# Performance work log

Hardware: AMD Instinct MI355X
Metric: run time of the kernel (lower is better)

Reference implementation:

```python
import jax, jax.numpy as jnp
import numpy as np

B, T, C = 128, 256, 384
H, HD = 8, 48          # num_heads, head_dim
WINDOW = 64

def setup_inputs() -> dict:
    key = jax.random.key(0)
    ks = jax.random.split(key, 5)
    return {
        "x": jax.random.normal(ks[0], (B, T, C), dtype=jnp.float32),
        "W_qkv": jax.random.normal(ks[1], (C, 3 * C), dtype=jnp.float32) * (1.0 / np.sqrt(C)),
        "b_qkv": jax.random.normal(ks[2], (3 * C,), dtype=jnp.float32) * 0.02,
        "W_proj": jax.random.normal(ks[3], (C, C), dtype=jnp.float32) * (1.0 / np.sqrt(C)),
        "b_proj": jax.random.normal(ks[4], (C,), dtype=jnp.float32) * 0.02,
        "gate": jnp.ones((C,), dtype=jnp.float32),
    }

def reference(x, W_qkv, b_qkv, W_proj, b_proj, gate):
    Bx, Tx, Cx = x.shape
    qkv = x @ W_qkv + b_qkv                                   # [B,T,3C]
    q, k, v = jnp.split(qkv, 3, axis=-1)
    q = q.reshape(Bx, Tx, H, HD).transpose(0, 2, 1, 3)        # [B,H,T,hd]
    k = k.reshape(Bx, Tx, H, HD).transpose(0, 2, 1, 3)
    v = v.reshape(Bx, Tx, H, HD).transpose(0, 2, 1, 3)
    scale = 1.0 / np.sqrt(HD).astype(np.float32)
    att = jnp.einsum("bhqd,bhkd->bhqk", q, k) * scale        # [B,H,T,T]
    idx = jnp.arange(Tx)
    causal = idx[:, None] >= idx[None, :]                     # lower-tri
    local = jnp.abs(idx[None, :] - idx[:, None]) <= WINDOW
    mask = (causal & local)[None, None, :, :]
    att = jnp.where(mask, att, -jnp.inf)
    att = jax.nn.softmax(att, axis=-1)
    out = jnp.einsum("bhqk,bhkd->bhqd", att, v)               # [B,H,T,hd]
    out = out.transpose(0, 2, 1, 3).reshape(Bx, Tx, Cx)       # [B,T,C]
    return (out * gate) @ W_proj + b_proj
```

## Files before the change

kernel.cpp:

```cpp
#include <hip/hip_runtime.h>
#include <hip/hip_bf16.h>

typedef __attribute__((ext_vector_type(8))) short bf16x8;
typedef __attribute__((ext_vector_type(4))) float floatx4;

#define NB 128
#define NT 256
#define NC 384
#define NH 8
#define ND 48

static __device__ __forceinline__ unsigned short f2bf(float f) {
  __hip_bfloat16 h = __float2bfloat16(f);
  return __builtin_bit_cast(unsigned short, h);
}

static __device__ __forceinline__ void gload16(const unsigned short* g, unsigned short* l) {
  __builtin_amdgcn_global_load_lds(
      (const __attribute__((address_space(1))) void*)g,
      (__attribute__((address_space(3))) void*)l, 16, 0, 0);
}

__global__ __launch_bounds__(256) void k_prep(const float* __restrict__ x,
                                              const float* __restrict__ Wq,
                                              const float* __restrict__ Wp,
                                              unsigned short* __restrict__ xbf,
                                              unsigned short* __restrict__ WqT,
                                              unsigned short* __restrict__ WpT) {
  const int blk = blockIdx.x;
  const int t = threadIdx.x;
  if (blk < 144) {
    __shared__ float T[64][65];
    const float* src;
    unsigned short* dst;
    int N, kt, nt;
    if (blk < 108) { src = Wq; dst = WqT; N = 1152; kt = blk / 18; nt = blk % 18; }
    else { int b2 = blk - 108; src = Wp; dst = WpT; N = 384; kt = b2 / 6; nt = b2 % 6; }
    const int k0 = kt * 64, n0 = nt * 64;
    const int r = t >> 2, c = (t & 3) * 16;
    const float* s = src + (size_t)(k0 + r) * N + n0 + c;
#pragma unroll
    for (int i = 0; i < 4; ++i) *(float4*)&T[r][c + i * 4] = ((const float4*)s)[i];
    __syncthreads();
    unsigned short o[16];
#pragma unroll
    for (int i = 0; i < 16; ++i) o[i] = f2bf(T[c + i][r]);
    unsigned short* dp = dst + (size_t)(n0 + r) * 384 + k0 + c;
    *(bf16x8*)dp = *(bf16x8*)&o[0];
    *(bf16x8*)(dp + 8) = *(bf16x8*)&o[8];
  } else {
    const int n8 = (NB * NT * NC) / 8;
    int idx = (blk - 144) * 256 + t;
    const int stride = (gridDim.x - 144) * 256;
    for (; idx < n8; idx += stride) {
      const float* s = x + (size_t)idx * 8;
      float v[8];
      *(float4*)&v[0] = ((const float4*)s)[0];
      *(float4*)&v[4] = ((const float4*)s)[1];
      bf16x8 p;
#pragma unroll
      for (int i = 0; i < 8; ++i) p[i] = f2bf(v[i]);
      *(bf16x8*)(xbf + (size_t)idx * 8) = p;
    }
  }
}

#define STAGE_G(Ag, Bg, As, Bs, k0, buf)                                             \
  {                                                                                  \
    const int r0_ = (lane >> 2), sw0_ = 8 * ((lane & 3) ^ ((r0_ >> 1) & 3));         \
    const int r1_ = r0_ + 16,    sw1_ = 8 * ((lane & 3) ^ ((r1_ >> 1) & 3));         \
    gload16(Ag + (size_t)r0_ * 384 + (k0) + sw0_, As + (buf)*4096 + (w * 32) * 32);  \
    gload16(Ag + (size_t)r1_ * 384 + (k0) + sw1_, As + (buf)*4096 + (w * 32 + 16) * 32); \
    gload16(Bg + (size_t)r0_ * 384 + (k0) + sw0_, Bs + (buf)*4096 + (w * 32) * 32);  \
    gload16(Bg + (size_t)r1_ * 384 + (k0) + sw1_, Bs + (buf)*4096 + (w * 32 + 16) * 32); \
  }

#define GEMM_PIPE(Ag, Bg, As, Bs)                                                    \
  STAGE_G(Ag, Bg, As, Bs, 0, 0);                                                     \
  STAGE_G(Ag, Bg, As, Bs, 32, 1);                                                    \
  _Pragma("unroll") for (int t_ = 0; t_ < 12; ++t_) {                                \
    if (t_ < 11) asm volatile("s_waitcnt vmcnt(4)" ::: "memory");                    \
    else         asm volatile("s_waitcnt vmcnt(0)" ::: "memory");                    \
    __builtin_amdgcn_s_barrier();                                                    \
    if (t_ < 10) STAGE_G(Ag, Bg, As, Bs, (t_ + 2) * 32, (t_ + 2) % 3);               \
    const unsigned short* Ac_ = As + (t_ % 3) * 4096;                                \
    const unsigned short* Bc_ = Bs + (t_ % 3) * 4096;                                \
    bf16x8 a_[4], b_[4];                                                             \
    _Pragma("unroll") for (int mt = 0; mt < 4; ++mt) {                               \
      const int R = wm * 64 + mt * 16 + lq;                                          \
      a_[mt] = *(const bf16x8*)&Ac_[R * 32 + 8 * (lg ^ ((R >> 1) & 3))];             \
    }                                                                                \
    _Pragma("unroll") for (int nt = 0; nt < 4; ++nt) {                               \
      const int R = wn * 64 + nt * 16 + lq;                                          \
      b_[nt] = *(const bf16x8*)&Bc_[R * 32 + 8 * (lg ^ ((R >> 1) & 3))];             \
    }                                                                                \
    _Pragma("unroll") for (int mt = 0; mt < 4; ++mt)                                 \
      _Pragma("unroll") for (int nt = 0; nt < 4; ++nt)                               \
        acc[mt][nt] = __builtin_amdgcn_mfma_f32_16x16x32_bf16(a_[mt], b_[nt], acc[mt][nt], 0, 0, 0); \
  }

__global__ __launch_bounds__(256) void k_qkv(const unsigned short* __restrict__ xb,
                                             const unsigned short* __restrict__ WqT,
                                             const float* __restrict__ bq,
                                             unsigned short* __restrict__ qkv) {
  __shared__ __align__(16) unsigned short As[3 * 128 * 32];
  __shared__ __align__(16) unsigned short Bs[3 * 128 * 32];
  const int t = threadIdx.x, lane = t & 63, w = t >> 6;
  const int wm = w >> 1, wn = w & 1;
  const int lq = lane & 15, lg = lane >> 4;
  const int m0 = blockIdx.x * 128, n0 = blockIdx.y * 128;
  const unsigned short* Ag = xb + (size_t)(m0 + w * 32) * 384;
  const unsigned short* Bg = WqT + (size_t)(n0 + w * 32) * 384;
  floatx4 acc[4][4] = {};

  GEMM_PIPE(Ag, Bg, As, Bs);

  const int comp = n0 / 384;
  const int cb = n0 - comp * 384;
#pragma unroll
  for (int nt = 0; nt < 4; ++nt) {
    const int cc = cb + wn * 64 + nt * 16 + lq;
    const int h = cc / 48, d = cc - h * 48;
    const float bias = bq[n0 + wn * 64 + nt * 16 + lq];
#pragma unroll
    for (int mt = 0; mt < 4; ++mt) {
#pragma unroll
      for (int j = 0; j < 4; ++j) {
        const int row = m0 + wm * 64 + mt * 16 + lg * 4 + j;
        const int bb = row >> 8, tt = row & 255;
        qkv[((((size_t)comp * NB + bb) * NH + h) * NT + tt) * ND + d] =
            f2bf(acc[mt][nt][j] + bias);
      }
    }
  }
}

__global__ __launch_bounds__(256) void k_proj(const unsigned short* __restrict__ A,
                                              const unsigned short* __restrict__ WpT,
                                              const float* __restrict__ bp,
                                              float* __restrict__ out) {
  __shared__ __align__(16) unsigned short As[3 * 128 * 32];
  __shared__ __align__(16) unsigned short Bs[3 * 128 * 32];
  const int t = threadIdx.x, lane = t & 63, w = t >> 6;
  const int wm = w >> 1, wn = w & 1;
  const int lq = lane & 15, lg = lane >> 4;
  const int m0 = blockIdx.x * 128, n0 = blockIdx.y * 128;
  const unsigned short* Ag = A + (size_t)(m0 + w * 32) * 384;
  const unsigned short* Bg = WpT + (size_t)(n0 + w * 32) * 384;
  floatx4 acc[4][4] = {};

  GEMM_PIPE(Ag, Bg, As, Bs);

#pragma unroll
  for (int nt = 0; nt < 4; ++nt) {
    const int col = n0 + wn * 64 + nt * 16 + lq;
    const float bias = bp[col];
#pragma unroll
    for (int mt = 0; mt < 4; ++mt)
#pragma unroll
      for (int j = 0; j < 4; ++j) {
        const int row = m0 + wm * 64 + mt * 16 + lg * 4 + j;
        out[(size_t)row * 384 + col] = acc[mt][nt][j] + bias;
      }
  }
}

__global__ __launch_bounds__(256) void k_attn(const unsigned short* __restrict__ qkv,
                                              const float* __restrict__ gate,
                                              unsigned short* __restrict__ attg) {
  __shared__ __align__(16) unsigned short Ks[128 * 72];
  __shared__ __align__(16) unsigned short Vt[48 * 152];
  __shared__ __align__(16) unsigned short Ps[4 * 16 * 104];
  const int t = threadIdx.x;
  const int blk = blockIdx.x;
  const int tile = blk & 3;
  const int bh = blk >> 2;
  const int b = bh >> 3, h = bh & 7;
  const int base = tile * 64;
  const size_t kvoff = (size_t)bh * NT * ND;
  const unsigned short* qptr = qkv + kvoff;
  const unsigned short* kptr = qkv + (size_t)NB * NH * NT * ND + kvoff;
  const unsigned short* vptr = qkv + (size_t)2 * NB * NH * NT * ND + kvoff;

  if (t < 48) {
    bf16x8 z = {};
    *(bf16x8*)&Vt[t * 152 + 128] = z;
    *(bf16x8*)&Vt[t * 152 + 136] = z;
  }
  if (t < 128) {
    const int r = t, ka = base - 64 + r;
    unsigned short* dst = &Ks[r * 72];
    if (ka >= 0) {
      const unsigned short* src = kptr + (size_t)ka * ND;
#pragma unroll
      for (int i = 0; i < 6; ++i) *(bf16x8*)(dst + i * 8) = *(const bf16x8*)(src + i * 8);
      bf16x8 z = {};
      *(bf16x8*)(dst + 48) = z;
      *(bf16x8*)(dst + 56) = z;
    } else {
      bf16x8 z = {};
#pragma unroll
      for (int i = 0; i < 8; ++i) *(bf16x8*)(dst + i * 8) = z;
    }
  } else {
    const int r = t - 128, ka = base - 64 + r;
    if (ka >= 0) {
      const unsigned short* src = vptr + (size_t)ka * ND;
      bf16x8 vv[6];
#pragma unroll
      for (int i = 0; i < 6; ++i) vv[i] = *(const bf16x8*)(src + i * 8);
#pragma unroll
      for (int i = 0; i < 6; ++i)
#pragma unroll
        for (int j = 0; j < 8; ++j)
          Vt[(i * 8 + j) * 152 + r] = (unsigned short)vv[i][j];
    } else {
#pragma unroll
      for (int d = 0; d < 48; ++d) Vt[d * 152 + r] = 0;
    }
  }
  __syncthreads();

  const int lane = t & 63, w = t >> 6;
  const int lq = lane & 15, lg = lane >> 4;
  const int qs = base + w * 16;

  const unsigned short* qrow = qptr + (size_t)(qs + lq) * ND;
  bf16x8 aq0 = *(const bf16x8*)(qrow + lg * 8);
  bf16x8 aq1 = {};
  if (lg < 2) aq1 = *(const bf16x8*)(qrow + 32 + lg * 8);

  floatx4 s[5];
#pragma unroll
  for (int kt = 0; kt < 5; ++kt) {
    const unsigned short* kr = &Ks[(w * 16 + kt * 16 + lq) * 72];
    bf16x8 kb0 = *(const bf16x8*)(kr + lg * 8);
    bf16x8 kb1 = *(const bf16x8*)(kr + 32 + lg * 8);
    floatx4 z = {};
    z = __builtin_amdgcn_mfma_f32_16x16x32_bf16(aq0, kb0, z, 0, 0, 0);
    z = __builtin_amdgcn_mfma_f32_16x16x32_bf16(aq1, kb1, z, 0, 0, 0);
    s[kt] = z;
  }

  const float scale = 0.14433756729740643f;
  floatx4 pj[5];
#pragma unroll
  for (int j = 0; j < 4; ++j) {
    const int qa = qs + lg * 4 + j;
    float mx = -1e30f;
    float sv[5];
    bool ok[5];
#pragma unroll
    for (int kt = 0; kt < 5; ++kt) {
      const int ka = base - 64 + w * 16 + kt * 16 + lq;
      sv[kt] = s[kt][j] * scale;
      ok[kt] = (ka >= 0) && (ka <= qa) && (qa - ka <= 64);
      if (ok[kt]) mx = fmaxf(mx, sv[kt]);
    }
#pragma unroll
    for (int dd = 1; dd < 16; dd <<= 1) mx = fmaxf(mx, __shfl_xor(mx, dd));
    float sum = 0.f;
#pragma unroll
    for (int kt = 0; kt < 5; ++kt) {
      float p = ok[kt] ? __expf(sv[kt] - mx) : 0.f;
      pj[kt][j] = p;
      sum += p;
    }
#pragma unroll
    for (int dd = 1; dd < 16; dd <<= 1) sum += __shfl_xor(sum, dd);
    const float inv = 1.f / sum;
#pragma unroll
    for (int kt = 0; kt < 5; ++kt) pj[kt][j] *= inv;
  }

  unsigned short* pw = &Ps[w * 16 * 104];
#pragma unroll
  for (int kt = 0; kt < 5; ++kt)
#pragma unroll
    for (int j = 0; j < 4; ++j)
      pw[(lg * 4 + j) * 104 + kt * 16 + lq] = f2bf(pj[kt][j]);
#pragma unroll
  for (int j = 0; j < 4; ++j) pw[lq * 104 + 80 + lg * 4 + j] = 0;

  floatx4 o[3] = {};
#pragma unroll
  for (int c = 0; c < 3; ++c) {
    bf16x8 ap = *(const bf16x8*)&pw[lq * 104 + c * 32 + lg * 8];
#pragma unroll
    for (int nt = 0; nt < 3; ++nt) {
      bf16x8 av = *(const bf16x8*)&Vt[(nt * 16 + lq) * 152 + w * 16 + c * 32 + lg * 8];
      o[nt] = __builtin_amdgcn_mfma_f32_16x16x32_bf16(ap, av, o[nt], 0, 0, 0);
    }
  }
#pragma unroll
  for (int nt = 0; nt < 3; ++nt) {
    const int d = nt * 16 + lq;
    const int c = h * ND + d;
    const float g = gate[c];
#pragma unroll
    for (int j = 0; j < 4; ++j) {
      const int tt = qs + lg * 4 + j;
      attg[((size_t)b * NT + tt) * NC + c] = f2bf(o[nt][j] * g);
    }
  }
}

extern "C" void kernel_launch(void* const* d_in, const int* in_sizes, int n_in,
                              void* d_out, int out_size, void* d_ws, size_t ws_size,
                              hipStream_t stream) {
  const float* x    = (const float*)d_in[0];
  const float* Wq   = (const float*)d_in[1];
  const float* bq   = (const float*)d_in[2];
  const float* Wp   = (const float*)d_in[3];
  const float* bp   = (const float*)d_in[4];
  const float* gate = (const float*)d_in[5];

  const size_t nx = (size_t)NB * NT * NC;
  unsigned short* attg = (unsigned short*)d_ws;
  unsigned short* xbf  = attg + nx;
  unsigned short* qkvp = xbf + nx;
  unsigned short* WqT  = qkvp + (size_t)3 * NB * NH * NT * ND;
  unsigned short* WpT  = WqT + (size_t)384 * 1152;
  float* out = (float*)d_out;

  k_prep<<<dim3(1680), 256, 0, stream>>>(x, Wq, Wp, xbf, WqT, WpT);
  k_qkv<<<dim3(256, 9), 256, 0, stream>>>(xbf, WqT, bq, qkvp);
  k_attn<<<dim3(4096), 256, 0, stream>>>(qkvp, gate, attg);
  k_proj<<<dim3(256, 3), 256, 0, stream>>>(attg, WpT, bp, out);
}
```

Baseline: 117.7 us.

## Deepen GEMM pipeline, store QKV row-major, fold gate into projection weights

The shared GEMM pipeline goes from three to four LDS stages, with one extra prefetch in flight and wave priority raised around the MFMA block. The QKV epilogue now writes a plain row-major [B*T,1152] layout instead of scattering into per-head tensors, and the attention kernel reads Q/K/V with a 1152 stride. The gate multiply moves from the attention epilogue into the projection weight transpose in k_prep. These target vmem latency stalls and scattered stores, at the cost of more LDS per block (possible occupancy loss) and strided attention loads.

New measurement: 137.1 us. +16.5%, slower.

```diff
diff --git a/kernel.cpp b/kernel.cpp
--- a/kernel.cpp
+++ b/kernel.cpp
@@ -24,6 +24,7 @@
 __global__ __launch_bounds__(256) void k_prep(const float* __restrict__ x,
                                               const float* __restrict__ Wq,
                                               const float* __restrict__ Wp,
+                                              const float* __restrict__ gate,
                                               unsigned short* __restrict__ xbf,
                                               unsigned short* __restrict__ WqT,
                                               unsigned short* __restrict__ WpT) {
@@ -34,7 +35,8 @@
     const float* src;
     unsigned short* dst;
     int N, kt, nt;
-    if (blk < 108) { src = Wq; dst = WqT; N = 1152; kt = blk / 18; nt = blk % 18; }
+    const bool isWp = (blk >= 108);
+    if (!isWp) { src = Wq; dst = WqT; N = 1152; kt = blk / 18; nt = blk % 18; }
     else { int b2 = blk - 108; src = Wp; dst = WpT; N = 384; kt = b2 / 6; nt = b2 % 6; }
     const int k0 = kt * 64, n0 = nt * 64;
     const int r = t >> 2, c = (t & 3) * 16;
@@ -42,9 +44,17 @@
 #pragma unroll
     for (int i = 0; i < 4; ++i) *(float4*)&T[r][c + i * 4] = ((const float4*)s)[i];
     __syncthreads();
+    float gv[16];
+    if (isWp) {
+#pragma unroll
+      for (int i = 0; i < 4; ++i) *(float4*)&gv[i * 4] = ((const float4*)(gate + k0 + c))[i];
+    } else {
+#pragma unroll
+      for (int i = 0; i < 16; ++i) gv[i] = 1.f;
+    }
     unsigned short o[16];
 #pragma unroll
-    for (int i = 0; i < 16; ++i) o[i] = f2bf(T[c + i][r]);
+    for (int i = 0; i < 16; ++i) o[i] = f2bf(T[c + i][r] * gv[i]);
     unsigned short* dp = dst + (size_t)(n0 + r) * 384 + k0 + c;
     *(bf16x8*)dp = *(bf16x8*)&o[0];
     *(bf16x8*)(dp + 8) = *(bf16x8*)&o[8];
@@ -78,13 +88,15 @@
 #define GEMM_PIPE(Ag, Bg, As, Bs)                                                    \
   STAGE_G(Ag, Bg, As, Bs, 0, 0);                                                     \
   STAGE_G(Ag, Bg, As, Bs, 32, 1);                                                    \
+  STAGE_G(Ag, Bg, As, Bs, 64, 2);                                                    \
   _Pragma("unroll") for (int t_ = 0; t_ < 12; ++t_) {                                \
-    if (t_ < 11) asm volatile("s_waitcnt vmcnt(4)" ::: "memory");                    \
-    else         asm volatile("s_waitcnt vmcnt(0)" ::: "memory");                    \
+    if (t_ <= 9)       asm volatile("s_waitcnt vmcnt(8)" ::: "memory");              \
+    else if (t_ == 10) asm volatile("s_waitcnt vmcnt(4)" ::: "memory");              \
+    else               asm volatile("s_waitcnt vmcnt(0)" ::: "memory");              \
     __builtin_amdgcn_s_barrier();                                                    \
-    if (t_ < 10) STAGE_G(Ag, Bg, As, Bs, (t_ + 2) * 32, (t_ + 2) % 3);               \
-    const unsigned short* Ac_ = As + (t_ % 3) * 4096;                                \
-    const unsigned short* Bc_ = Bs + (t_ % 3) * 4096;                                \
+    if (t_ < 9) STAGE_G(Ag, Bg, As, Bs, (t_ + 3) * 32, (t_ + 3) & 3);                \
+    const unsigned short* Ac_ = As + (t_ & 3) * 4096;                                \
+    const unsigned short* Bc_ = Bs + (t_ & 3) * 4096;                                \
     bf16x8 a_[4], b_[4];                                                             \
     _Pragma("unroll") for (int mt = 0; mt < 4; ++mt) {                               \
       const int R = wm * 64 + mt * 16 + lq;                                          \
@@ -94,17 +106,19 @@
       const int R = wn * 64 + nt * 16 + lq;                                          \
       b_[nt] = *(const bf16x8*)&Bc_[R * 32 + 8 * (lg ^ ((R >> 1) & 3))];             \
     }                                                                                \
+    __builtin_amdgcn_s_setprio(1);                                                   \
     _Pragma("unroll") for (int mt = 0; mt < 4; ++mt)                                 \
       _Pragma("unroll") for (int nt = 0; nt < 4; ++nt)                               \
         acc[mt][nt] = __builtin_amdgcn_mfma_f32_16x16x32_bf16(a_[mt], b_[nt], acc[mt][nt], 0, 0, 0); \
+    __builtin_amdgcn_s_setprio(0);                                                   \
   }
 
 __global__ __launch_bounds__(256) void k_qkv(const unsigned short* __restrict__ xb,
                                              const unsigned short* __restrict__ WqT,
                                              const float* __restrict__ bq,
                                              unsigned short* __restrict__ qkv) {
-  __shared__ __align__(16) unsigned short As[3 * 128 * 32];
-  __shared__ __align__(16) unsigned short Bs[3 * 128 * 32];
+  __shared__ __align__(16) unsigned short As[4 * 128 * 32];
+  __shared__ __align__(16) unsigned short Bs[4 * 128 * 32];
   const int t = threadIdx.x, lane = t & 63, w = t >> 6;
   const int wm = w >> 1, wn = w & 1;
   const int lq = lane & 15, lg = lane >> 4;
@@ -115,23 +129,17 @@
 
   GEMM_PIPE(Ag, Bg, As, Bs);
 
-  const int comp = n0 / 384;
-  const int cb = n0 - comp * 384;
 #pragma unroll
   for (int nt = 0; nt < 4; ++nt) {
-    const int cc = cb + wn * 64 + nt * 16 + lq;
-    const int h = cc / 48, d = cc - h * 48;
-    const float bias = bq[n0 + wn * 64 + nt * 16 + lq];
-#pragma unroll
-    for (int mt = 0; mt < 4; ++mt) {
+    const int col = n0 + wn * 64 + nt * 16 + lq;
+    const float bias = bq[col];
+#pragma unroll
+    for (int mt = 0; mt < 4; ++mt)
 #pragma unroll
       for (int j = 0; j < 4; ++j) {
         const int row = m0 + wm * 64 + mt * 16 + lg * 4 + j;
-        const int bb = row >> 8, tt = row & 255;
-        qkv[((((size_t)comp * NB + bb) * NH + h) * NT + tt) * ND + d] =
-            f2bf(acc[mt][nt][j] + bias);
+        qkv[(size_t)row * 1152 + col] = f2bf(acc[mt][nt][j] + bias);
       }
-    }
   }
 }
 
@@ -139,8 +147,8 @@
                                               const unsigned short* __restrict__ WpT,
                                               const float* __restrict__ bp,
                                               float* __restrict__ out) {
-  __shared__ __align__(16) unsigned short As[3 * 128 * 32];
-  __shared__ __align__(16) unsigned short Bs[3 * 128 * 32];
+  __shared__ __align__(16) unsigned short As[4 * 128 * 32];
+  __shared__ __align__(16) unsigned short Bs[4 * 128 * 32];
   const int t = threadIdx.x, lane = t & 63, w = t >> 6;
   const int wm = w >> 1, wn = w & 1;
   const int lq = lane & 15, lg = lane >> 4;
@@ -166,7 +174,6 @@
 }
 
 __global__ __launch_bounds__(256) void k_attn(const unsigned short* __restrict__ qkv,
-                                              const float* __restrict__ gate,
                                               unsigned short* __restrict__ attg) {
   __shared__ __align__(16) unsigned short Ks[128 * 72];
   __shared__ __align__(16) unsigned short Vt[48 * 152];
@@ -177,10 +184,9 @@
   const int bh = blk >> 2;
   const int b = bh >> 3, h = bh & 7;
   const int base = tile * 64;
-  const size_t kvoff = (size_t)bh * NT * ND;
-  const unsigned short* qptr = qkv + kvoff;
-  const unsigned short* kptr = qkv + (size_t)NB * NH * NT * ND + kvoff;
-  const unsigned short* vptr = qkv + (size_t)2 * NB * NH * NT * ND + kvoff;
+  const unsigned short* qbase = qkv + (size_t)(b * NT) * 1152 + h * 48;
+  const unsigned short* kbase = qbase + 384;
+  const unsigned short* vbase = qbase + 768;
 
   if (t < 48) {
     bf16x8 z = {};
@@ -191,7 +197,7 @@
     const int r = t, ka = base - 64 + r;
     unsigned short* dst = &Ks[r * 72];
     if (ka >= 0) {
-      const unsigned short* src = kptr + (size_t)ka * ND;
+      const unsigned short* src = kbase + (size_t)ka * 1152;
 #pragma unroll
       for (int i = 0; i < 6; ++i) *(bf16x8*)(dst + i * 8) = *(const bf16x8*)(src + i * 8);
       bf16x8 z = {};
@@ -205,7 +211,7 @@
   } else {
     const int r = t - 128, ka = base - 64 + r;
     if (ka >= 0) {
-      const unsigned short* src = vptr + (size_t)ka * ND;
+      const unsigned short* src = vbase + (size_t)ka * 1152;
       bf16x8 vv[6];
 #pragma unroll
       for (int i = 0; i < 6; ++i) vv[i] = *(const bf16x8*)(src + i * 8);
@@ -225,7 +231,7 @@
   const int lq = lane & 15, lg = lane >> 4;
   const int qs = base + w * 16;
 
-  const unsigned short* qrow = qptr + (size_t)(qs + lq) * ND;
+  const unsigned short* qrow = qbase + (size_t)(qs + lq) * 1152;
   bf16x8 aq0 = *(const bf16x8*)(qrow + lg * 8);
   bf16x8 aq1 = {};
   if (lg < 2) aq1 = *(const bf16x8*)(qrow + 32 + lg * 8);
@@ -296,11 +302,10 @@
   for (int nt = 0; nt < 3; ++nt) {
     const int d = nt * 16 + lq;
     const int c = h * ND + d;
-    const float g = gate[c];
 #pragma unroll
     for (int j = 0; j < 4; ++j) {
       const int tt = qs + lg * 4 + j;
-      attg[((size_t)b * NT + tt) * NC + c] = f2bf(o[nt][j] * g);
+      attg[((size_t)b * NT + tt) * NC + c] = f2bf(o[nt][j]);
     }
   }
 }
@@ -319,12 +324,12 @@
   unsigned short* attg = (unsigned short*)d_ws;
   unsigned short* xbf  = attg + nx;
   unsigned short* qkvp = xbf + nx;
-  unsigned short* WqT  = qkvp + (size_t)3 * NB * NH * NT * ND;
+  unsigned short* WqT  = qkvp + (size_t)NB * NT * 1152;
   unsigned short* WpT  = WqT + (size_t)384 * 1152;
   float* out = (float*)d_out;
 
-  k_prep<<<dim3(1680), 256, 0, stream>>>(x, Wq, Wp, xbf, WqT, WpT);
+  k_prep<<<dim3(1680), 256, 0, stream>>>(x, Wq, Wp, gate, xbf, WqT, WpT);
   k_qkv<<<dim3(256, 9), 256, 0, stream>>>(xbf, WqT, bq, qkvp);
-  k_attn<<<dim3(4096), 256, 0, stream>>>(qkvp, gate, attg);
+  k_attn<<<dim3(4096), 256, 0, stream>>>(qkvp, attg);
   k_proj<<<dim3(256, 3), 256, 0, stream>>>(attg, WpT, bp, out);
 }
```
